# Kernel tuning notes

Measured on AMD Instinct MI355X. Metric: run time of the kernel, lower is better.

Reference implementation:

```python
import jax, jax.numpy as jnp
import numpy as np

N_NODES = 50000
N_EDGES = 600000
IN_F = 128
OUT_F = 128
SMALL = max(IN_F // 10, 1)  # floor(128/10) = 12
D_K = np.sqrt(SMALL).astype(np.float32)


def setup_inputs() -> dict:
    key = jax.random.key(0)
    ks = jax.random.split(key, 10)
    node_data = jax.random.normal(ks[0], (N_NODES, IN_F), dtype=jnp.float32)
    src = jax.random.randint(ks[1], (N_EDGES,), 0, N_NODES, dtype=jnp.int32)
    dst = jax.random.randint(ks[2], (N_EDGES,), 0, N_NODES, dtype=jnp.int32)
    s_q = 1.0 / np.sqrt(IN_F)
    Wq = jax.random.uniform(ks[3], (SMALL, IN_F), jnp.float32, -s_q, s_q)
    bq = jax.random.uniform(ks[4], (SMALL,), jnp.float32, -s_q, s_q)
    Wk = jax.random.uniform(ks[5], (SMALL, IN_F), jnp.float32, -s_q, s_q)
    bk = jax.random.uniform(ks[6], (SMALL,), jnp.float32, -s_q, s_q)
    W1 = jax.random.uniform(ks[7], (OUT_F, IN_F), jnp.float32, -s_q, s_q)
    W2 = jax.random.uniform(ks[8], (OUT_F, IN_F), jnp.float32, -s_q, s_q)
    b2 = jax.random.uniform(ks[9], (OUT_F,), jnp.float32, -s_q, s_q)
    return {"node_data": node_data, "src": src, "dst": dst,
            "Wq": Wq, "bq": bq, "Wk": Wk, "bk": bk,
            "W1": W1, "W2": W2, "b2": b2}


def reference(node_data, src, dst, Wq, bq, Wk, bk, W1, W2, b2):
    N = node_data.shape[0]
    # dgl.add_self_loop: append (i, i) for every node -> each dst has >= 1 edge
    loops = jnp.arange(N, dtype=src.dtype)
    s = jnp.concatenate([src, loops])
    d = jnp.concatenate([dst, loops])

    # query = Tanh(Linear), key = Linear  (shapes [N, SMALL])
    q = jnp.tanh(node_data @ Wq.T + bq)
    k = node_data @ Wk.T + bk

    # per-edge score: sum(query[src] * key[dst]) / sqrt(small)
    scores = jnp.sum(q[s] * k[d], axis=1) / D_K  # [E]

    # softmax over incoming edges of each dst node (segment softmax)
    seg_max = jax.ops.segment_max(scores, d, num_segments=N)
    w = jnp.exp(scores - seg_max[d])
    seg_sum = jax.ops.segment_sum(w, d, num_segments=N)
    w = w / seg_sum[d]  # [E]

    # weighted scatter-aggregate of src node inputs -> [N, IN_F]
    att = jax.ops.segment_sum(w[:, None] * node_data[s], d, num_segments=N)

    # DeepSetLayer: layer1(node_data) + layer2(node attention)
    x = node_data @ W1.T + (att @ W2.T + b2)
    # per-row L2 ('fro' over dim=1) normalization, then ReLU
    x = x / jnp.linalg.norm(x, axis=1, keepdims=True)
    return jax.nn.relu(x)
```

## Files before the change

kernel.cpp:

```cpp
#include <hip/hip_runtime.h>
#include <hip/hip_bf16.h>
#include <math.h>
#include <stdint.h>


#define IN_F 128
#define SMALL 12
#define QK_PAD 16
#define SCAN_ITEMS 8
#define SCAN_CHUNK 2048
#define ALD 136

typedef __attribute__((ext_vector_type(8))) short short8;
typedef __attribute__((ext_vector_type(4))) float f32x4;

__device__ __forceinline__ unsigned short f2bf(float f) {
    union { float f; unsigned u; } v; v.f = f;
    unsigned r = v.u + 0x7fff + ((v.u >> 16) & 1);
    return (unsigned short)(r >> 16);
}

__device__ __forceinline__ float2 bf2x2(unsigned v) {
    union { unsigned u; float f; } a, b;
    a.u = v << 16;
    b.u = v & 0xffff0000u;
    return make_float2(a.f, b.f);
}

__device__ __forceinline__ float dot12(const float* __restrict__ qrow,
                                       float4 c0, float4 c1, float4 c2) {
    float4 a = ((const float4*)qrow)[0];
    float4 b = ((const float4*)qrow)[1];
    float4 c = ((const float4*)qrow)[2];
    return a.x*c0.x + a.y*c0.y + a.z*c0.z + a.w*c0.w
         + b.x*c1.x + b.y*c1.y + b.z*c1.z + b.w*c1.w
         + c.x*c2.x + c.y*c2.y + c.z*c2.z + c.w*c2.w;
}

__device__ __forceinline__ short8 ld_bf8(const float* p) {
    float4 x0 = *(const float4*)p;
    float4 x1 = *(const float4*)(p + 4);
    short8 a;
    a[0] = (short)f2bf(x0.x); a[1] = (short)f2bf(x0.y);
    a[2] = (short)f2bf(x0.z); a[3] = (short)f2bf(x0.w);
    a[4] = (short)f2bf(x1.x); a[5] = (short)f2bf(x1.y);
    a[6] = (short)f2bf(x1.z); a[7] = (short)f2bf(x1.w);
    return a;
}

__global__ __launch_bounds__(256) void prep_kernel(
    const float* __restrict__ nd,
    const float* __restrict__ Wq, const float* __restrict__ bq,
    const float* __restrict__ Wk, const float* __restrict__ bk,
    const int* __restrict__ dst,
    const float* __restrict__ W1, const float* __restrict__ W2,
    float* __restrict__ q, float* __restrict__ kf,
    unsigned short* __restrict__ ndb, int* __restrict__ cnt,
    unsigned short* __restrict__ rank, unsigned short* __restrict__ Wc,
    int N, int E, int NBQK, int NBCNT)
{
    int t = threadIdx.x;
    int b = blockIdx.x;

    if (b < NBQK) {
        int wv = t >> 6;
        int lane = t & 63;
        int col = lane & 15;
        int quad = lane >> 4;
        int tbase = b * 64 + wv * 16;

        int arow = tbase + col;
        int rowc = (arow < N) ? arow : (N - 1);
        const float* ap = nd + (size_t)rowc * IN_F + quad * 8;
        unsigned short* np = ndb + (size_t)arow * IN_F + quad * 8;

        const float* w0 = ((col < 12) ? (Wq + (size_t)col * IN_F)
                                      : (Wk + (size_t)(col - 12) * IN_F)) + quad * 8;
        const float* w1 = Wk + (size_t)((col < 8) ? (col + 4) : 4) * IN_F + quad * 8;
        bool hasw1 = (col < 8);

        f32x4 acc0 = (f32x4)0.f, acc1 = (f32x4)0.f;
#pragma unroll
        for (int ks = 0; ks < 4; ks++) {
            int k0 = ks * 32;
            short8 a = ld_bf8(ap + k0);
            if (arow < N) *(short8*)(np + k0) = a;
            short8 bb0 = ld_bf8(w0 + k0);
            short8 bb1 = hasw1 ? ld_bf8(w1 + k0) : (short8)0;
            acc0 = __builtin_amdgcn_mfma_f32_16x16x32_bf16(a, bb0, acc0, 0, 0, 0);
            acc1 = __builtin_amdgcn_mfma_f32_16x16x32_bf16(a, bb1, acc1, 0, 0, 0);
        }
        float bias0 = (col < 12) ? bq[col] : bk[col - 12];
        float bias1 = (col < 8) ? bk[col + 4] : 0.f;
#pragma unroll
        for (int r = 0; r < 4; r++) {
            int node = tbase + quad * 4 + r;
            if (node < N) {
                float v0 = acc0[r] + bias0;
                if (col < 12) q[(size_t)node * QK_PAD + col] = tanhf(v0);
                else          kf[(size_t)node * QK_PAD + (col - 12)] = v0;
                if (hasw1)    kf[(size_t)node * QK_PAD + col + 4] = acc1[r] + bias1;
            }
        }
    } else if (b < NBQK + NBCNT) {
        int ET = E + N;
        int stride = NBCNT * 256;
        for (int i = (b - NBQK) * 256 + t; i < ET; i += stride) {
            int d = (i < E) ? dst[i] : (i - E);
            rank[i] = (unsigned short)atomicAdd(&cnt[d], 1);
        }
    } else {
        int idx = (b - NBQK - NBCNT) * 256 + t;
        int f = idx >> 8, k = idx & 255;
        float v = (k < 128) ? W1[f * 128 + k] : W2[f * 128 + (k - 128)];
        Wc[idx] = f2bf(v);
    }
}

__global__ __launch_bounds__(256) void scan_local_kernel(
    int* __restrict__ off, int* __restrict__ bsum, int N)
{
    __shared__ int tsum[256];
    int t = threadIdx.x;
    int base = blockIdx.x * SCAN_CHUNK + t * SCAN_ITEMS;
    int v[SCAN_ITEMS];
    int s = 0;
#pragma unroll
    for (int i = 0; i < SCAN_ITEMS; i++) {
        int idx = base + i;
        v[i] = (idx < N) ? off[idx] : 0;
        s += v[i];
    }
    tsum[t] = s;
    __syncthreads();
    for (int d = 1; d < 256; d <<= 1) {
        int x = (t >= d) ? tsum[t - d] : 0;
        __syncthreads();
        tsum[t] += x;
        __syncthreads();
    }
    int excl = (t == 0) ? 0 : tsum[t - 1];
#pragma unroll
    for (int i = 0; i < SCAN_ITEMS; i++) {
        int idx = base + i;
        if (idx < N) off[idx] = excl;
        excl += v[i];
    }
    if (t == 255) bsum[blockIdx.x] = tsum[255];
}

__global__ __launch_bounds__(256) void scan_add_kernel(
    int* __restrict__ off, const int* __restrict__ bsum, int N, int NB)
{
    __shared__ int pre2[2];
    int t = threadIdx.x;
    if (t == 0) {
        int p = 0, tot = 0;
        for (int i = 0; i < NB; i++) {
            int v = bsum[i];
            if (i < (int)blockIdx.x) p += v;
            tot += v;
        }
        pre2[0] = p; pre2[1] = tot;
    }
    __syncthreads();
    int add = pre2[0];
    if (blockIdx.x == 0 && t == 0) off[N] = pre2[1];

    int base = blockIdx.x * SCAN_CHUNK + t * SCAN_ITEMS;
#pragma unroll
    for (int i = 0; i < SCAN_ITEMS; i++) {
        int j = base + i;
        if (j < N) off[j] += add;
    }
}

__global__ __launch_bounds__(256) void scatter_kernel(
    const int* __restrict__ src, const int* __restrict__ dst,
    const int* __restrict__ off, const unsigned short* __restrict__ rank,
    unsigned short* __restrict__ esrc, int E, int N)
{
    int i = blockIdx.x * 256 + threadIdx.x;
    if (i >= E + N) return;
    int d, s;
    if (i < E) { d = dst[i]; s = src[i]; }
    else       { d = i - E; s = d; }
    esrc[off[d] + (int)rank[i]] = (unsigned short)s;
}

__global__ __launch_bounds__(256) void attn_final_kernel(
    const unsigned short* __restrict__ ndb, const float* __restrict__ q,
    const float* __restrict__ kf, const int* __restrict__ off,
    const unsigned short* __restrict__ esrc,
    const unsigned short* __restrict__ Wc, const float* __restrict__ b2,
    float* __restrict__ out, int N)
{
    __shared__ unsigned short att_lds[64][ALD];

    const float INVDK = 0.28867513459481287f;
    int t = threadIdx.x;
    int wv = t >> 6;
    int lane = t & 63;
    int col = lane & 15;
    int quad = lane >> 4;
    int nbase = blockIdx.x * 64;

    for (int it = 0; it < 16; it++) {
        int wid = nbase + wv * 16 + it;
        if (wid >= N) break;

        int start = off[wid];
        int deg = off[wid + 1] - start;

        const float4* kp = (const float4*)(kf + (size_t)wid * QK_PAD);
        float4 c0 = kp[0], c1 = kp[1], c2 = kp[2];

        float2 acc = make_float2(0.f, 0.f);
        float inv;

        if (deg <= 64) {
            float sc = -INFINITY;
            int si = 0;
            if (lane < deg) {
                si = (int)esrc[start + lane];
                sc = dot12(q + (size_t)si * QK_PAD, c0, c1, c2) * INVDK;
            }
            float m = sc;
#pragma unroll
            for (int o = 32; o > 0; o >>= 1) m = fmaxf(m, __shfl_xor(m, o));
            float w = (lane < deg) ? __expf(sc - m) : 0.f;
            float lsum = w;
#pragma unroll
            for (int o = 32; o > 0; o >>= 1) lsum += __shfl_xor(lsum, o);
            inv = 1.f / lsum;

            int i = 0;
            for (; i + 4 <= deg; i += 4) {
                float w0 = __shfl(w, i);     int r0 = __shfl(si, i);
                float w1 = __shfl(w, i + 1); int r1 = __shfl(si, i + 1);
                float w2 = __shfl(w, i + 2); int r2 = __shfl(si, i + 2);
                float w3 = __shfl(w, i + 3); int r3 = __shfl(si, i + 3);
                unsigned v0 = *(const unsigned*)(ndb + (size_t)r0 * IN_F + lane * 2);
                unsigned v1 = *(const unsigned*)(ndb + (size_t)r1 * IN_F + lane * 2);
                unsigned v2 = *(const unsigned*)(ndb + (size_t)r2 * IN_F + lane * 2);
                unsigned v3 = *(const unsigned*)(ndb + (size_t)r3 * IN_F + lane * 2);
                float2 f0 = bf2x2(v0), f1 = bf2x2(v1), f2 = bf2x2(v2), f3 = bf2x2(v3);
                acc.x += w0 * f0.x + w1 * f1.x + w2 * f2.x + w3 * f3.x;
                acc.y += w0 * f0.y + w1 * f1.y + w2 * f2.y + w3 * f3.y;
            }
            for (; i < deg; i++) {
                float wi = __shfl(w, i);
                int r = __shfl(si, i);
                float2 f = bf2x2(*(const unsigned*)(ndb + (size_t)r * IN_F + lane * 2));
                acc.x += wi * f.x;
                acc.y += wi * f.y;
            }
        } else {
            float m = -INFINITY;
            for (int i = lane; i < deg; i += 64) {
                int s2 = (int)esrc[start + i];
                m = fmaxf(m, dot12(q + (size_t)s2 * QK_PAD, c0, c1, c2) * INVDK);
            }
#pragma unroll
            for (int o = 32; o > 0; o >>= 1) m = fmaxf(m, __shfl_xor(m, o));
            float lsum = 0.f;
            for (int i = lane; i < deg; i += 64) {
                int s2 = (int)esrc[start + i];
                lsum += __expf(dot12(q + (size_t)s2 * QK_PAD, c0, c1, c2) * INVDK - m);
            }
#pragma unroll
            for (int o = 32; o > 0; o >>= 1) lsum += __shfl_xor(lsum, o);
            inv = 1.f / lsum;
            for (int base2 = 0; base2 < deg; base2 += 64) {
                int cnt2 = deg - base2; if (cnt2 > 64) cnt2 = 64;
                float w = 0.f; int si = 0;
                if (lane < cnt2) {
                    si = (int)esrc[start + base2 + lane];
                    w = __expf(dot12(q + (size_t)si * QK_PAD, c0, c1, c2) * INVDK - m);
                }
                for (int i = 0; i < cnt2; i++) {
                    float wi = __shfl(w, i);
                    int r = __shfl(si, i);
                    float2 f = bf2x2(*(const unsigned*)(ndb + (size_t)r * IN_F + lane * 2));
                    acc.x += wi * f.x;
                    acc.y += wi * f.y;
                }
            }
        }
        acc.x *= inv; acc.y *= inv;
        unsigned pak = (unsigned)f2bf(acc.x) | ((unsigned)f2bf(acc.y) << 16);
        *(unsigned*)&att_lds[wv * 16 + it][lane * 2] = pak;
    }
    __syncthreads();

    int arow = nbase + wv * 16 + col;
    int rowc = (arow < N) ? arow : (N - 1);
    const unsigned short* a0p = ndb + (size_t)rowc * IN_F + quad * 8;
    const unsigned short* alp = &att_lds[wv * 16 + col][quad * 8];

    f32x4 acc[8];
#pragma unroll
    for (int i = 0; i < 8; i++) acc[i] = (f32x4)0.f;

#pragma unroll
    for (int ks = 0; ks < 8; ks++) {
        int k0 = ks * 32;
        short8 a;
        if (ks < 4) a = *(const short8*)(a0p + k0);
        else        a = *(const short8*)(alp + (k0 - 128));
#pragma unroll
        for (int ft = 0; ft < 8; ft++) {
            int n = ft * 16 + col;
            short8 bb = *(const short8*)(Wc + (size_t)n * 256 + k0 + quad * 8);
            acc[ft] = __builtin_amdgcn_mfma_f32_16x16x32_bf16(a, bb, acc[ft], 0, 0, 0);
        }
    }

    float bias[8];
#pragma unroll
    for (int ft = 0; ft < 8; ft++) bias[ft] = b2[ft * 16 + col];

#pragma unroll
    for (int r = 0; r < 4; r++) {
        int node = nbase + wv * 16 + quad * 4 + r;
        float v[8];
        float ps = 0.f;
#pragma unroll
        for (int ft = 0; ft < 8; ft++) {
            v[ft] = acc[ft][r] + bias[ft];
            ps += v[ft] * v[ft];
        }
        ps += __shfl_xor(ps, 1);
        ps += __shfl_xor(ps, 2);
        ps += __shfl_xor(ps, 4);
        ps += __shfl_xor(ps, 8);
        float rn = rsqrtf(ps);
        if (node < N) {
            float* op = out + (size_t)node * 128 + col;
#pragma unroll
            for (int ft = 0; ft < 8; ft++)
                op[ft * 16] = fmaxf(v[ft] * rn, 0.f);
        }
    }
}

static inline char* align_up(char* p, size_t a) {
    return (char*)(((uintptr_t)p + (a - 1)) & ~(uintptr_t)(a - 1));
}

extern "C" void kernel_launch(void* const* d_in, const int* in_sizes, int n_in,
                              void* d_out, int out_size, void* d_ws, size_t ws_size,
                              hipStream_t stream) {
    const float* node_data = (const float*)d_in[0];
    const int*   src       = (const int*)d_in[1];
    const int*   dst       = (const int*)d_in[2];
    const float* Wq        = (const float*)d_in[3];
    const float* bq        = (const float*)d_in[4];
    const float* Wk        = (const float*)d_in[5];
    const float* bk        = (const float*)d_in[6];
    const float* W1        = (const float*)d_in[7];
    const float* W2        = (const float*)d_in[8];
    const float* b2        = (const float*)d_in[9];
    float* out = (float*)d_out;

    int N = in_sizes[0] / IN_F;
    int E = in_sizes[1];
    int ET = E + N;
    int NB = (N + SCAN_CHUNK - 1) / SCAN_CHUNK;
    int NBQK = (N + 63) / 64;
    int NBCNT = 512;
    int NBCVT = 128;
    int NT = (N + 63) / 64;

    char* w = (char*)d_ws;
    float* q  = (float*)w;  w += (size_t)N * QK_PAD * sizeof(float);
    float* kf = (float*)w;  w += (size_t)N * QK_PAD * sizeof(float);
    w = align_up(w, 256);
    unsigned short* ndb = (unsigned short*)w;  w += (size_t)N * IN_F * sizeof(unsigned short);
    w = align_up(w, 256);
    unsigned short* Wc = (unsigned short*)w;  w += 128 * 256 * sizeof(unsigned short);
    int* off  = (int*)w;  w += (size_t)(N + 1) * sizeof(int);
    int* bsum = (int*)w;  w += 256 * sizeof(int);
    unsigned short* rank = (unsigned short*)w;  w += (size_t)ET * sizeof(unsigned short);
    w = align_up(w, 256);
    unsigned short* esrc = (unsigned short*)w;  w += (size_t)ET * sizeof(unsigned short);

    hipMemsetAsync(off, 0, (size_t)(N + 1) * sizeof(int), stream);

    prep_kernel<<<NBQK + NBCNT + NBCVT, 256, 0, stream>>>(
        node_data, Wq, bq, Wk, bk, dst, W1, W2,
        q, kf, ndb, off, rank, Wc, N, E, NBQK, NBCNT);
    scan_local_kernel<<<NB, 256, 0, stream>>>(off, bsum, N);
    scan_add_kernel<<<NB, 256, 0, stream>>>(off, bsum, N, NB);
    scatter_kernel<<<(ET + 255) / 256, 256, 0, stream>>>(src, dst, off, rank, esrc, E, N);
    attn_final_kernel<<<NT, 256, 0, stream>>>(ndb, q, kf, off, esrc, Wc, b2, out, N);
}
```

Baseline: 231.8 us.

## Split fused attention kernel into weights, column-sliced aggregation and final GEMM kernels

The single attention-plus-output kernel is broken into three launches. The first computes normalized softmax edge weights into a per-edge buffer. The second aggregates neighbour features, with each block handling one 16-column slice and 8 edges processed in parallel per wave, and writes fp32 attention rows into the output buffer as scratch. The third runs the MFMA projection and normalization from that buffer. The goal is better parallelism and load balance in the gather, in exchange for extra global round-trips for the weights and the fp32 attention matrix, plus narrow 4-byte gathers per slice.

```diff
diff --git a/kernel.cpp b/kernel.cpp
--- a/kernel.cpp
+++ b/kernel.cpp
@@ -9,7 +9,6 @@
 #define QK_PAD 16
 #define SCAN_ITEMS 8
 #define SCAN_CHUNK 2048
-#define ALD 136
 
 typedef __attribute__((ext_vector_type(8))) short short8;
 typedef __attribute__((ext_vector_type(4))) float f32x4;
@@ -188,115 +187,121 @@
     esrc[off[d] + (int)rank[i]] = (unsigned short)s;
 }
 
-__global__ __launch_bounds__(256) void attn_final_kernel(
-    const unsigned short* __restrict__ ndb, const float* __restrict__ q,
-    const float* __restrict__ kf, const int* __restrict__ off,
-    const unsigned short* __restrict__ esrc,
+__global__ __launch_bounds__(256) void weights_kernel(
+    const float* __restrict__ q, const float* __restrict__ kf,
+    const int* __restrict__ off, const unsigned short* __restrict__ esrc,
+    float* __restrict__ wn, int N)
+{
+    const float INVDK = 0.28867513459481287f;
+    int wid = blockIdx.x * 4 + (threadIdx.x >> 6);
+    if (wid >= N) return;
+    int lane = threadIdx.x & 63;
+
+    int start = off[wid];
+    int deg = off[wid + 1] - start;
+
+    const float4* kp = (const float4*)(kf + (size_t)wid * QK_PAD);
+    float4 c0 = kp[0], c1 = kp[1], c2 = kp[2];
+
+    if (deg <= 64) {
+        float sc = -INFINITY;
+        if (lane < deg) {
+            int si = (int)esrc[start + lane];
+            sc = dot12(q + (size_t)si * QK_PAD, c0, c1, c2) * INVDK;
+        }
+        float m = sc;
+#pragma unroll
+        for (int o = 32; o > 0; o >>= 1) m = fmaxf(m, __shfl_xor(m, o));
+        float w = (lane < deg) ? __expf(sc - m) : 0.f;
+        float lsum = w;
+#pragma unroll
+        for (int o = 32; o > 0; o >>= 1) lsum += __shfl_xor(lsum, o);
+        float inv = 1.f / lsum;
+        if (lane < deg) wn[start + lane] = w * inv;
+    } else {
+        float m = -INFINITY;
+        for (int i = lane; i < deg; i += 64) {
+            int s2 = (int)esrc[start + i];
+            m = fmaxf(m, dot12(q + (size_t)s2 * QK_PAD, c0, c1, c2) * INVDK);
+        }
+#pragma unroll
+        for (int o = 32; o > 0; o >>= 1) m = fmaxf(m, __shfl_xor(m, o));
+        float lsum = 0.f;
+        for (int i = lane; i < deg; i += 64) {
+            int s2 = (int)esrc[start + i];
+            lsum += __expf(dot12(q + (size_t)s2 * QK_PAD, c0, c1, c2) * INVDK - m);
+        }
+#pragma unroll
+        for (int o = 32; o > 0; o >>= 1) lsum += __shfl_xor(lsum, o);
+        float inv = 1.f / lsum;
+        for (int i = lane; i < deg; i += 64) {
+            int s2 = (int)esrc[start + i];
+            wn[start + i] = __expf(dot12(q + (size_t)s2 * QK_PAD, c0, c1, c2) * INVDK - m) * inv;
+        }
+    }
+}
+
+__global__ __launch_bounds__(256) void agg_kernel(
+    const unsigned short* __restrict__ ndb, const int* __restrict__ off,
+    const unsigned short* __restrict__ esrc, const float* __restrict__ wn,
+    float* __restrict__ att, int N, int NBB)
+{
+    int slice = blockIdx.x & 7;
+    int bs = blockIdx.x >> 3;
+    int wv = threadIdx.x >> 6;
+    int lane = threadIdx.x & 63;
+    int eg = lane >> 3;
+    int fp = lane & 7;
+    int bcol = slice * 16 + fp * 2;
+
+    for (int wid = bs * 4 + wv; wid < N; wid += NBB * 4) {
+        int start = off[wid];
+        int deg = off[wid + 1] - start;
+
+        float ax = 0.f, ay = 0.f;
+        int i = eg;
+        for (; i + 8 < deg; i += 16) {
+            int e0 = start + i, e1 = start + i + 8;
+            int r0 = (int)esrc[e0];
+            int r1 = (int)esrc[e1];
+            float w0 = wn[e0];
+            float w1 = wn[e1];
+            float2 f0 = bf2x2(*(const unsigned*)(ndb + (size_t)r0 * IN_F + bcol));
+            float2 f1 = bf2x2(*(const unsigned*)(ndb + (size_t)r1 * IN_F + bcol));
+            ax += w0 * f0.x + w1 * f1.x;
+            ay += w0 * f0.y + w1 * f1.y;
+        }
+        if (i < deg) {
+            int e0 = start + i;
+            int r0 = (int)esrc[e0];
+            float w0 = wn[e0];
+            float2 f0 = bf2x2(*(const unsigned*)(ndb + (size_t)r0 * IN_F + bcol));
+            ax += w0 * f0.x;
+            ay += w0 * f0.y;
+        }
+        ax += __shfl_xor(ax, 8);  ay += __shfl_xor(ay, 8);
+        ax += __shfl_xor(ax, 16); ay += __shfl_xor(ay, 16);
+        ax += __shfl_xor(ax, 32); ay += __shfl_xor(ay, 32);
+        if (eg == 0)
+            *(float2*)(att + (size_t)wid * IN_F + bcol) = make_float2(ax, ay);
+    }
+}
+
+__global__ __launch_bounds__(256) void final_kernel(
+    const unsigned short* __restrict__ ndb, const float* __restrict__ nd,
+    const float* __restrict__ att,
     const unsigned short* __restrict__ Wc, const float* __restrict__ b2,
     float* __restrict__ out, int N)
 {
-    __shared__ unsigned short att_lds[64][ALD];
-
-    const float INVDK = 0.28867513459481287f;
-    int t = threadIdx.x;
-    int wv = t >> 6;
-    int lane = t & 63;
+    int wv = threadIdx.x >> 6;
+    int lane = threadIdx.x & 63;
     int col = lane & 15;
     int quad = lane >> 4;
-    int nbase = blockIdx.x * 64;
-
-    for (int it = 0; it < 16; it++) {
-        int wid = nbase + wv * 16 + it;
-        if (wid >= N) break;
-
-        int start = off[wid];
-        int deg = off[wid + 1] - start;
-
-        const float4* kp = (const float4*)(kf + (size_t)wid * QK_PAD);
-        float4 c0 = kp[0], c1 = kp[1], c2 = kp[2];
-
-        float2 acc = make_float2(0.f, 0.f);
-        float inv;
-
-        if (deg <= 64) {
-            float sc = -INFINITY;
-            int si = 0;
-            if (lane < deg) {
-                si = (int)esrc[start + lane];
-                sc = dot12(q + (size_t)si * QK_PAD, c0, c1, c2) * INVDK;
-            }
-            float m = sc;
-#pragma unroll
-            for (int o = 32; o > 0; o >>= 1) m = fmaxf(m, __shfl_xor(m, o));
-            float w = (lane < deg) ? __expf(sc - m) : 0.f;
-            float lsum = w;
-#pragma unroll
-            for (int o = 32; o > 0; o >>= 1) lsum += __shfl_xor(lsum, o);
-            inv = 1.f / lsum;
-
-            int i = 0;
-            for (; i + 4 <= deg; i += 4) {
-                float w0 = __shfl(w, i);     int r0 = __shfl(si, i);
-                float w1 = __shfl(w, i + 1); int r1 = __shfl(si, i + 1);
-                float w2 = __shfl(w, i + 2); int r2 = __shfl(si, i + 2);
-                float w3 = __shfl(w, i + 3); int r3 = __shfl(si, i + 3);
-                unsigned v0 = *(const unsigned*)(ndb + (size_t)r0 * IN_F + lane * 2);
-                unsigned v1 = *(const unsigned*)(ndb + (size_t)r1 * IN_F + lane * 2);
-                unsigned v2 = *(const unsigned*)(ndb + (size_t)r2 * IN_F + lane * 2);
-                unsigned v3 = *(const unsigned*)(ndb + (size_t)r3 * IN_F + lane * 2);
-                float2 f0 = bf2x2(v0), f1 = bf2x2(v1), f2 = bf2x2(v2), f3 = bf2x2(v3);
-                acc.x += w0 * f0.x + w1 * f1.x + w2 * f2.x + w3 * f3.x;
-                acc.y += w0 * f0.y + w1 * f1.y + w2 * f2.y + w3 * f3.y;
-            }
-            for (; i < deg; i++) {
-                float wi = __shfl(w, i);
-                int r = __shfl(si, i);
-                float2 f = bf2x2(*(const unsigned*)(ndb + (size_t)r * IN_F + lane * 2));
-                acc.x += wi * f.x;
-                acc.y += wi * f.y;
-            }
-        } else {
-            float m = -INFINITY;
-            for (int i = lane; i < deg; i += 64) {
-                int s2 = (int)esrc[start + i];
-                m = fmaxf(m, dot12(q + (size_t)s2 * QK_PAD, c0, c1, c2) * INVDK);
-            }
-#pragma unroll
-            for (int o = 32; o > 0; o >>= 1) m = fmaxf(m, __shfl_xor(m, o));
-            float lsum = 0.f;
-            for (int i = lane; i < deg; i += 64) {
-                int s2 = (int)esrc[start + i];
-                lsum += __expf(dot12(q + (size_t)s2 * QK_PAD, c0, c1, c2) * INVDK - m);
-            }
-#pragma unroll
-            for (int o = 32; o > 0; o >>= 1) lsum += __shfl_xor(lsum, o);
-            inv = 1.f / lsum;
-            for (int base2 = 0; base2 < deg; base2 += 64) {
-                int cnt2 = deg - base2; if (cnt2 > 64) cnt2 = 64;
-                float w = 0.f; int si = 0;
-                if (lane < cnt2) {
-                    si = (int)esrc[start + base2 + lane];
-                    w = __expf(dot12(q + (size_t)si * QK_PAD, c0, c1, c2) * INVDK - m);
-                }
-                for (int i = 0; i < cnt2; i++) {
-                    float wi = __shfl(w, i);
-                    int r = __shfl(si, i);
-                    float2 f = bf2x2(*(const unsigned*)(ndb + (size_t)r * IN_F + lane * 2));
-                    acc.x += wi * f.x;
-                    acc.y += wi * f.y;
-                }
-            }
-        }
-        acc.x *= inv; acc.y *= inv;
-        unsigned pak = (unsigned)f2bf(acc.x) | ((unsigned)f2bf(acc.y) << 16);
-        *(unsigned*)&att_lds[wv * 16 + it][lane * 2] = pak;
-    }
-    __syncthreads();
-
-    int arow = nbase + wv * 16 + col;
+
+    int arow = blockIdx.x * 64 + wv * 16 + col;
     int rowc = (arow < N) ? arow : (N - 1);
     const unsigned short* a0p = ndb + (size_t)rowc * IN_F + quad * 8;
-    const unsigned short* alp = &att_lds[wv * 16 + col][quad * 8];
+    const float* a1p = ((arow < N) ? att : nd) + (size_t)rowc * IN_F + quad * 8;
 
     f32x4 acc[8];
 #pragma unroll
@@ -307,7 +312,7 @@
         int k0 = ks * 32;
         short8 a;
         if (ks < 4) a = *(const short8*)(a0p + k0);
-        else        a = *(const short8*)(alp + (k0 - 128));
+        else        a = ld_bf8(a1p + (k0 - 128));
 #pragma unroll
         for (int ft = 0; ft < 8; ft++) {
             int n = ft * 16 + col;
@@ -322,7 +327,7 @@
 
 #pragma unroll
     for (int r = 0; r < 4; r++) {
-        int node = nbase + wv * 16 + quad * 4 + r;
+        int node = blockIdx.x * 64 + wv * 16 + quad * 4 + r;
         float v[8];
         float ps = 0.f;
 #pragma unroll
@@ -370,7 +375,7 @@
     int NBQK = (N + 63) / 64;
     int NBCNT = 512;
     int NBCVT = 128;
-    int NT = (N + 63) / 64;
+    int NBB = (N + 31) / 32;
 
     char* w = (char*)d_ws;
     float* q  = (float*)w;  w += (size_t)N * QK_PAD * sizeof(float);
@@ -381,9 +386,11 @@
     unsigned short* Wc = (unsigned short*)w;  w += 128 * 256 * sizeof(unsigned short);
     int* off  = (int*)w;  w += (size_t)(N + 1) * sizeof(int);
     int* bsum = (int*)w;  w += 256 * sizeof(int);
+    float* wn = (float*)w;  w += (size_t)ET * sizeof(float);
     unsigned short* rank = (unsigned short*)w;  w += (size_t)ET * sizeof(unsigned short);
     w = align_up(w, 256);
     unsigned short* esrc = (unsigned short*)w;  w += (size_t)ET * sizeof(unsigned short);
+    float* att = out;
 
     hipMemsetAsync(off, 0, (size_t)(N + 1) * sizeof(int), stream);
 
@@ -393,5 +400,7 @@
     scan_local_kernel<<<NB, 256, 0, stream>>>(off, bsum, N);
     scan_add_kernel<<<NB, 256, 0, stream>>>(off, bsum, N, NB);
     scatter_kernel<<<(ET + 255) / 256, 256, 0, stream>>>(src, dst, off, rank, esrc, E, N);
-    attn_final_kernel<<<NT, 256, 0, stream>>>(ndb, q, kf, off, esrc, Wc, b2, out, N);
-}
+    weights_kernel<<<(N + 3) / 4, 256, 0, stream>>>(q, kf, off, esrc, wn, N);
+    agg_kernel<<<NBB * 8, 256, 0, stream>>>(ndb, off, esrc, wn, att, N, NBB);
+    final_kernel<<<(N + 63) / 64, 256, 0, stream>>>(ndb, node_data, att, Wc, b2, out, N);
+}
```

Result: slower. 298.9 us (+29.0%).

## Split attention and output GEMM, use 16-lane groups per node for gather

Applied to the files above, without the earlier changes.

The fused attention-plus-GEMM kernel is split into two kernels. The attention kernel now gives each destination node 16 lanes instead of a full 64-lane wave, and gathers neighbour rows with 16-byte loads. This fits the average in-degree (about 13) much better and should raise lane utilisation and memory-level parallelism. The cost is that the fp32 attention result makes a round trip through the output buffer before final_kernel reads it back. final_kernel then overwrites the same buffer in place, which is correct only because each wave reads and writes the same rows.

```diff
diff --git a/kernel.cpp b/kernel.cpp
--- a/kernel.cpp
+++ b/kernel.cpp
@@ -9,7 +9,6 @@
 #define QK_PAD 16
 #define SCAN_ITEMS 8
 #define SCAN_CHUNK 2048
-#define ALD 136
 
 typedef __attribute__((ext_vector_type(8))) short short8;
 typedef __attribute__((ext_vector_type(4))) float f32x4;
@@ -188,115 +187,144 @@
     esrc[off[d] + (int)rank[i]] = (unsigned short)s;
 }
 
-__global__ __launch_bounds__(256) void attn_final_kernel(
+__global__ __launch_bounds__(256) void attn_kernel(
     const unsigned short* __restrict__ ndb, const float* __restrict__ q,
     const float* __restrict__ kf, const int* __restrict__ off,
-    const unsigned short* __restrict__ esrc,
+    const unsigned short* __restrict__ esrc, float* __restrict__ att, int N)
+{
+    const float INVDK = 0.28867513459481287f;
+    int t = threadIdx.x;
+    int lane = t & 63;
+    int l16 = lane & 15;
+    int gbase = lane & 48;
+    int wid = blockIdx.x * 16 + (t >> 4);
+    if (wid >= N) return;
+
+    int start = off[wid];
+    int deg = off[wid + 1] - start;
+
+    const float4* kp = (const float4*)(kf + (size_t)wid * QK_PAD);
+    float4 c0 = kp[0], c1 = kp[1], c2 = kp[2];
+
+    float acc[8];
+#pragma unroll
+    for (int j = 0; j < 8; j++) acc[j] = 0.f;
+    float inv;
+
+    const unsigned short* nb = ndb + l16 * 8;
+
+#define ACCUM(vv, ww) do {                                                    \
+        float2 f0 = bf2x2((vv).x), f1 = bf2x2((vv).y);                        \
+        float2 f2 = bf2x2((vv).z), f3 = bf2x2((vv).w);                        \
+        acc[0] += (ww) * f0.x; acc[1] += (ww) * f0.y;                         \
+        acc[2] += (ww) * f1.x; acc[3] += (ww) * f1.y;                         \
+        acc[4] += (ww) * f2.x; acc[5] += (ww) * f2.y;                         \
+        acc[6] += (ww) * f3.x; acc[7] += (ww) * f3.y;                         \
+    } while (0)
+
+    if (deg <= 16) {
+        float sc = -INFINITY;
+        int si = 0;
+        if (l16 < deg) {
+            si = (int)esrc[start + l16];
+            sc = dot12(q + (size_t)si * QK_PAD, c0, c1, c2) * INVDK;
+        }
+        float m = sc;
+#pragma unroll
+        for (int o = 8; o > 0; o >>= 1) m = fmaxf(m, __shfl_xor(m, o));
+        float w = (l16 < deg) ? __expf(sc - m) : 0.f;
+        float ls = w;
+#pragma unroll
+        for (int o = 8; o > 0; o >>= 1) ls += __shfl_xor(ls, o);
+        inv = 1.f / ls;
+
+        int i = 0;
+        for (; i + 4 <= deg; i += 4) {
+            float w0 = __shfl(w, gbase | i);       int r0 = __shfl(si, gbase | i);
+            float w1 = __shfl(w, gbase | (i + 1)); int r1 = __shfl(si, gbase | (i + 1));
+            float w2 = __shfl(w, gbase | (i + 2)); int r2 = __shfl(si, gbase | (i + 2));
+            float w3 = __shfl(w, gbase | (i + 3)); int r3 = __shfl(si, gbase | (i + 3));
+            uint4 v0 = *(const uint4*)(nb + (size_t)r0 * IN_F);
+            uint4 v1 = *(const uint4*)(nb + (size_t)r1 * IN_F);
+            uint4 v2 = *(const uint4*)(nb + (size_t)r2 * IN_F);
+            uint4 v3 = *(const uint4*)(nb + (size_t)r3 * IN_F);
+            ACCUM(v0, w0); ACCUM(v1, w1); ACCUM(v2, w2); ACCUM(v3, w3);
+        }
+        for (; i < deg; i++) {
+            float wi = __shfl(w, gbase | i);
+            int ri = __shfl(si, gbase | i);
+            uint4 v = *(const uint4*)(nb + (size_t)ri * IN_F);
+            ACCUM(v, wi);
+        }
+    } else {
+        float m = -INFINITY;
+        for (int i = l16; i < deg; i += 16) {
+            int s2 = (int)esrc[start + i];
+            m = fmaxf(m, dot12(q + (size_t)s2 * QK_PAD, c0, c1, c2) * INVDK);
+        }
+#pragma unroll
+        for (int o = 8; o > 0; o >>= 1) m = fmaxf(m, __shfl_xor(m, o));
+        float ls = 0.f;
+        for (int i = l16; i < deg; i += 16) {
+            int s2 = (int)esrc[start + i];
+            ls += __expf(dot12(q + (size_t)s2 * QK_PAD, c0, c1, c2) * INVDK - m);
+        }
+#pragma unroll
+        for (int o = 8; o > 0; o >>= 1) ls += __shfl_xor(ls, o);
+        inv = 1.f / ls;
+
+        for (int base2 = 0; base2 < deg; base2 += 16) {
+            int cnt2 = deg - base2; if (cnt2 > 16) cnt2 = 16;
+            float w = 0.f; int si = 0;
+            if (l16 < cnt2) {
+                si = (int)esrc[start + base2 + l16];
+                w = __expf(dot12(q + (size_t)si * QK_PAD, c0, c1, c2) * INVDK - m);
+            }
+            int i = 0;
+            for (; i + 4 <= cnt2; i += 4) {
+                float w0 = __shfl(w, gbase | i);       int r0 = __shfl(si, gbase | i);
+                float w1 = __shfl(w, gbase | (i + 1)); int r1 = __shfl(si, gbase | (i + 1));
+                float w2 = __shfl(w, gbase | (i + 2)); int r2 = __shfl(si, gbase | (i + 2));
+                float w3 = __shfl(w, gbase | (i + 3)); int r3 = __shfl(si, gbase | (i + 3));
+                uint4 v0 = *(const uint4*)(nb + (size_t)r0 * IN_F);
+                uint4 v1 = *(const uint4*)(nb + (size_t)r1 * IN_F);
+                uint4 v2 = *(const uint4*)(nb + (size_t)r2 * IN_F);
+                uint4 v3 = *(const uint4*)(nb + (size_t)r3 * IN_F);
+                ACCUM(v0, w0); ACCUM(v1, w1); ACCUM(v2, w2); ACCUM(v3, w3);
+            }
+            for (; i < cnt2; i++) {
+                float wi = __shfl(w, gbase | i);
+                int ri = __shfl(si, gbase | i);
+                uint4 v = *(const uint4*)(nb + (size_t)ri * IN_F);
+                ACCUM(v, wi);
+            }
+        }
+    }
+#undef ACCUM
+
+    float* op = att + (size_t)wid * IN_F + l16 * 8;
+    float4 s0, s1;
+    s0.x = acc[0] * inv; s0.y = acc[1] * inv; s0.z = acc[2] * inv; s0.w = acc[3] * inv;
+    s1.x = acc[4] * inv; s1.y = acc[5] * inv; s1.z = acc[6] * inv; s1.w = acc[7] * inv;
+    *(float4*)op = s0;
+    *(float4*)(op + 4) = s1;
+}
+
+__global__ __launch_bounds__(256) void final_kernel(
+    const unsigned short* __restrict__ ndb, const float* __restrict__ nd,
+    const float* __restrict__ att,
     const unsigned short* __restrict__ Wc, const float* __restrict__ b2,
     float* __restrict__ out, int N)
 {
-    __shared__ unsigned short att_lds[64][ALD];
-
-    const float INVDK = 0.28867513459481287f;
-    int t = threadIdx.x;
-    int wv = t >> 6;
-    int lane = t & 63;
+    int wv = threadIdx.x >> 6;
+    int lane = threadIdx.x & 63;
     int col = lane & 15;
     int quad = lane >> 4;
-    int nbase = blockIdx.x * 64;
-
-    for (int it = 0; it < 16; it++) {
-        int wid = nbase + wv * 16 + it;
-        if (wid >= N) break;
-
-        int start = off[wid];
-        int deg = off[wid + 1] - start;
-
-        const float4* kp = (const float4*)(kf + (size_t)wid * QK_PAD);
-        float4 c0 = kp[0], c1 = kp[1], c2 = kp[2];
-
-        float2 acc = make_float2(0.f, 0.f);
-        float inv;
-
-        if (deg <= 64) {
-            float sc = -INFINITY;
-            int si = 0;
-            if (lane < deg) {
-                si = (int)esrc[start + lane];
-                sc = dot12(q + (size_t)si * QK_PAD, c0, c1, c2) * INVDK;
-            }
-            float m = sc;
-#pragma unroll
-            for (int o = 32; o > 0; o >>= 1) m = fmaxf(m, __shfl_xor(m, o));
-            float w = (lane < deg) ? __expf(sc - m) : 0.f;
-            float lsum = w;
-#pragma unroll
-            for (int o = 32; o > 0; o >>= 1) lsum += __shfl_xor(lsum, o);
-            inv = 1.f / lsum;
-
-            int i = 0;
-            for (; i + 4 <= deg; i += 4) {
-                float w0 = __shfl(w, i);     int r0 = __shfl(si, i);
-                float w1 = __shfl(w, i + 1); int r1 = __shfl(si, i + 1);
-                float w2 = __shfl(w, i + 2); int r2 = __shfl(si, i + 2);
-                float w3 = __shfl(w, i + 3); int r3 = __shfl(si, i + 3);
-                unsigned v0 = *(const unsigned*)(ndb + (size_t)r0 * IN_F + lane * 2);
-                unsigned v1 = *(const unsigned*)(ndb + (size_t)r1 * IN_F + lane * 2);
-                unsigned v2 = *(const unsigned*)(ndb + (size_t)r2 * IN_F + lane * 2);
-                unsigned v3 = *(const unsigned*)(ndb + (size_t)r3 * IN_F + lane * 2);
-                float2 f0 = bf2x2(v0), f1 = bf2x2(v1), f2 = bf2x2(v2), f3 = bf2x2(v3);
-                acc.x += w0 * f0.x + w1 * f1.x + w2 * f2.x + w3 * f3.x;
-                acc.y += w0 * f0.y + w1 * f1.y + w2 * f2.y + w3 * f3.y;
-            }
-            for (; i < deg; i++) {
-                float wi = __shfl(w, i);
-                int r = __shfl(si, i);
-                float2 f = bf2x2(*(const unsigned*)(ndb + (size_t)r * IN_F + lane * 2));
-                acc.x += wi * f.x;
-                acc.y += wi * f.y;
-            }
-        } else {
-            float m = -INFINITY;
-            for (int i = lane; i < deg; i += 64) {
-                int s2 = (int)esrc[start + i];
-                m = fmaxf(m, dot12(q + (size_t)s2 * QK_PAD, c0, c1, c2) * INVDK);
-            }
-#pragma unroll
-            for (int o = 32; o > 0; o >>= 1) m = fmaxf(m, __shfl_xor(m, o));
-            float lsum = 0.f;
-            for (int i = lane; i < deg; i += 64) {
-                int s2 = (int)esrc[start + i];
-                lsum += __expf(dot12(q + (size_t)s2 * QK_PAD, c0, c1, c2) * INVDK - m);
-            }
-#pragma unroll
-            for (int o = 32; o > 0; o >>= 1) lsum += __shfl_xor(lsum, o);
-            inv = 1.f / lsum;
-            for (int base2 = 0; base2 < deg; base2 += 64) {
-                int cnt2 = deg - base2; if (cnt2 > 64) cnt2 = 64;
-                float w = 0.f; int si = 0;
-                if (lane < cnt2) {
-                    si = (int)esrc[start + base2 + lane];
-                    w = __expf(dot12(q + (size_t)si * QK_PAD, c0, c1, c2) * INVDK - m);
-                }
-                for (int i = 0; i < cnt2; i++) {
-                    float wi = __shfl(w, i);
-                    int r = __shfl(si, i);
-                    float2 f = bf2x2(*(const unsigned*)(ndb + (size_t)r * IN_F + lane * 2));
-                    acc.x += wi * f.x;
-                    acc.y += wi * f.y;
-                }
-            }
-        }
-        acc.x *= inv; acc.y *= inv;
-        unsigned pak = (unsigned)f2bf(acc.x) | ((unsigned)f2bf(acc.y) << 16);
-        *(unsigned*)&att_lds[wv * 16 + it][lane * 2] = pak;
-    }
-    __syncthreads();
-
-    int arow = nbase + wv * 16 + col;
+
+    int arow = blockIdx.x * 64 + wv * 16 + col;
     int rowc = (arow < N) ? arow : (N - 1);
     const unsigned short* a0p = ndb + (size_t)rowc * IN_F + quad * 8;
-    const unsigned short* alp = &att_lds[wv * 16 + col][quad * 8];
+    const float* a1p = ((arow < N) ? att : nd) + (size_t)rowc * IN_F + quad * 8;
 
     f32x4 acc[8];
 #pragma unroll
@@ -307,7 +335,7 @@
         int k0 = ks * 32;
         short8 a;
         if (ks < 4) a = *(const short8*)(a0p + k0);
-        else        a = *(const short8*)(alp + (k0 - 128));
+        else        a = ld_bf8(a1p + (k0 - 128));
 #pragma unroll
         for (int ft = 0; ft < 8; ft++) {
             int n = ft * 16 + col;
@@ -322,7 +350,7 @@
 
 #pragma unroll
     for (int r = 0; r < 4; r++) {
-        int node = nbase + wv * 16 + quad * 4 + r;
+        int node = blockIdx.x * 64 + wv * 16 + quad * 4 + r;
         float v[8];
         float ps = 0.f;
 #pragma unroll
@@ -370,7 +398,6 @@
     int NBQK = (N + 63) / 64;
     int NBCNT = 512;
     int NBCVT = 128;
-    int NT = (N + 63) / 64;
 
     char* w = (char*)d_ws;
     float* q  = (float*)w;  w += (size_t)N * QK_PAD * sizeof(float);
@@ -384,6 +411,7 @@
     unsigned short* rank = (unsigned short*)w;  w += (size_t)ET * sizeof(unsigned short);
     w = align_up(w, 256);
     unsigned short* esrc = (unsigned short*)w;  w += (size_t)ET * sizeof(unsigned short);
+    float* att = out;
 
     hipMemsetAsync(off, 0, (size_t)(N + 1) * sizeof(int), stream);
 
@@ -393,5 +421,6 @@
     scan_local_kernel<<<NB, 256, 0, stream>>>(off, bsum, N);
     scan_add_kernel<<<NB, 256, 0, stream>>>(off, bsum, N, NB);
     scatter_kernel<<<(ET + 255) / 256, 256, 0, stream>>>(src, dst, off, rank, esrc, E, N);
-    attn_final_kernel<<<NT, 256, 0, stream>>>(ndb, q, kf, off, esrc, Wc, b2, out, N);
-}
+    attn_kernel<<<(N + 15) / 16, 256, 0, stream>>>(ndb, q, kf, off, esrc, att, N);
+    final_kernel<<<(N + 63) / 64, 256, 0, stream>>>(ndb, node_data, att, Wc, b2, out, N);
+}
```

After: 220.5 us. -4.9%, faster.
